# Performance work log

Measured on AMD Instinct MI355X. Metric: run time of the kernel, lower is better.

The kernel has to match this reference:

```python
import jax, jax.numpy as jnp
import numpy as np

LRELU_GAIN = np.sqrt(2.0).astype(np.float32)  # apply_activation gain for leaky_relu


def setup_inputs() -> dict:
    key = jax.random.key(0)
    ks = jax.random.split(key, 8)
    N, H, W, C_in = 8, 256, 256, 128
    num_ws, w_dim, fmaps, kernel = 16, 512, 128, 3
    return {
        "x": jax.random.normal(ks[0], (N, H, W, C_in), dtype=jnp.float32),
        "dlatents": jax.random.normal(ks[1], (N, num_ws, w_dim), dtype=jnp.float32),
        "noise": jax.random.normal(ks[2], (N, H, W, 1), dtype=jnp.float32),
        "affine_w": jax.random.normal(ks[3], (w_dim, C_in), dtype=jnp.float32),
        "affine_b": jnp.ones((C_in,), dtype=jnp.float32),  # bias_init=1
        "conv_w": jax.random.normal(ks[4], (kernel, kernel, C_in, fmaps), dtype=jnp.float32),
        "conv_b": jax.random.normal(ks[5], (fmaps,), dtype=jnp.float32),
        "noise_strength": jax.random.uniform(ks[6], (1,), dtype=jnp.float32),
        "layer_idx": 5,
    }


def reference(x, dlatents, noise, affine_w, affine_b, conv_w, conv_b, noise_strength, layer_idx):
    # --- affine (equalized-lr Linear, lr_multiplier=1): s = z @ (W/sqrt(fan_in)) + b ---
    w_dim = affine_w.shape[0]
    z = dlatents[:, layer_idx]                                   # [N, w_dim]
    s = z @ (affine_w * np.float32(1.0 / np.sqrt(w_dim))) + affine_b   # [N, C_in]

    # --- equalized-lr conv weight: w * 1/sqrt(k*k*C_in) ---
    k, _, cin, cout = conv_w.shape
    w = conv_w * np.float32(1.0 / np.sqrt(k * k * cin))          # [k,k,Cin,Cout]

    # --- demodulation coefficient d[n,o] = rsqrt(sum_{k,k,i} (w*s)^2 + eps) ---
    d = jax.lax.rsqrt(jnp.einsum('hwio,ni->no', jnp.square(w), jnp.square(s)) + 1e-8)  # [N, Cout]

    # --- non-fused modconv: modulate input, shared conv, demodulate output ---
    xm = x * s[:, None, None, :]                                 # [N,H,W,Cin]
    y = jax.lax.conv_general_dilated(
        xm, w, window_strides=(1, 1), padding='SAME',
        dimension_numbers=('NHWC', 'HWIO', 'NHWC'))              # [N,H,W,Cout]
    y = y * d[:, None, None, :]

    # --- noise injection, bias, activation (leaky_relu 0.2 with sqrt(2) gain) ---
    y = y + noise_strength[0] * noise
    y = y + conv_b
    return jax.nn.leaky_relu(y, negative_slope=0.2) * LRELU_GAIN
```

## Files before the change

### kernel.cpp

```cpp
#include <hip/hip_runtime.h>

typedef unsigned short u16;
typedef unsigned int   u32;
typedef __bf16 v8bf __attribute__((ext_vector_type(8)));
typedef float  v4f  __attribute__((ext_vector_type(4)));

#define INV_SQRT_W   0.044194173824159216f
#define INV_SQRT_KKC 0.029462782549439483f
#define LRELU_GAIN   1.4142135623730951f

__device__ __forceinline__ u16 f2bf(float f) {
    u32 u = __float_as_uint(f);
    u = (u + 0x7fffu + ((u >> 16) & 1u)) >> 16;
    return (u16)u;
}

__global__ void k_s(const float* __restrict__ dlat,
                    const float* __restrict__ aw,
                    const float* __restrict__ ab,
                    const int*   __restrict__ lidx,
                    float* __restrict__ s_out)
{
    const int n   = blockIdx.x;
    const int tid = threadIdx.x;
    const int i   = tid & 127, kh = tid >> 7;
    const int li  = lidx[0];
    const float* z = dlat + (n * 16 + li) * 512 + kh * 256;
    const float* a = aw + kh * 256 * 128 + i;
    float a0 = 0.f, a1 = 0.f, a2 = 0.f, a3 = 0.f;
    for (int k = 0; k < 256; k += 4) {
        a0 += z[k + 0] * a[(k + 0) * 128];
        a1 += z[k + 1] * a[(k + 1) * 128];
        a2 += z[k + 2] * a[(k + 2) * 128];
        a3 += z[k + 3] * a[(k + 3) * 128];
    }
    __shared__ float part[256];
    part[tid] = a0 + a1 + a2 + a3;
    __syncthreads();
    if (tid < 128)
        s_out[n * 128 + i] = (part[i] + part[i + 128]) * INV_SQRT_W + ab[i];
}

__global__ void k_w2(const float* __restrict__ cw, float* __restrict__ W2)
{
    const int idx = blockIdx.x * 256 + threadIdx.x;
    float acc = 0.f;
    #pragma unroll
    for (int t = 0; t < 9; ++t) {
        float w = cw[t * 16384 + idx];
        acc += w * w;
    }
    W2[idx] = acc * (INV_SQRT_KKC * INV_SQRT_KKC);
}

__global__ void k_d(const float* __restrict__ W2,
                    const float* __restrict__ s_buf,
                    float* __restrict__ d_out)
{
    const int n = blockIdx.x;
    const int o = threadIdx.x;
    __shared__ float s2[128];
    float sv = s_buf[n * 128 + o];
    s2[o] = sv * sv;
    __syncthreads();
    float acc = 1e-8f;
    #pragma unroll 4
    for (int i = 0; i < 128; ++i)
        acc += W2[i * 128 + o] * s2[i];
    d_out[n * 128 + o] = 1.0f / sqrtf(acc);
}

__global__ void k_wmod(const float* __restrict__ cw,
                       const float* __restrict__ s_buf,
                       const float* __restrict__ d_buf,
                       u16* __restrict__ wmod)
{
    const int b   = blockIdx.x;
    const int n   = b / 36;
    const int s   = b - n * 36;
    const int q4  = s / 9;
    const int r   = s - q4 * 9;
    const int tw  = r / 3, th = r - tw * 3;
    const int tap = th * 3 + tw;
    const int cibase = q4 * 32;
    const int tid = threadIdx.x;
    __shared__ float ssh[32], dsh[128];
    if (tid < 32)  ssh[tid] = s_buf[n * 128 + cibase + tid] * INV_SQRT_KKC;
    if (tid < 128) dsh[tid] = d_buf[n * 128 + tid];
    __syncthreads();
    u16* wt = wmod + ((size_t)b << 12);
    #pragma unroll
    for (int rep = 0; rep < 2; ++rep) {
        int t2   = rep * 256 + tid;
        int g    = t2 >> 7;
        int cout = t2 & 127;
        float dv = dsh[cout];
        u32 pk[4];
        #pragma unroll
        for (int jj = 0; jj < 4; ++jj) {
            int cl = g * 8 + jj * 2;
            float v0 = cw[((tap * 128 + cibase + cl) << 7) + cout]     * ssh[cl]     * dv;
            float v1 = cw[((tap * 128 + cibase + cl + 1) << 7) + cout] * ssh[cl + 1] * dv;
            pk[jj] = (u32)f2bf(v0) | ((u32)f2bf(v1) << 16);
        }
        *(uint4*)&wt[(g << 10) + (cout << 3)] = *(uint4*)pk;
    }
}

template<int T>
__device__ __forceinline__ void conv_step(const u16* __restrict__ bp,
                                          const u16* a_base,
                                          v8bf af[6], v8bf bfP[2][4],
                                          v4f acc[4][4])
{
    constexpr int q4 = T / 9, rr = T % 9, tw = rr / 3, th = rr % 3;
    constexpr int slot = T & 1;
    if constexpr (th == 0) {
        #pragma unroll
        for (int r = 0; r < 6; ++r)
            af[r] = *(const v8bf*)(a_base + q4 * 5824 + (r * 18 + tw) * 8);
    }
    #pragma unroll
    for (int mi = 0; mi < 4; ++mi)
        #pragma unroll
        for (int ni = 0; ni < 4; ++ni)
            acc[mi][ni] = __builtin_amdgcn_mfma_f32_16x16x32_bf16(
                af[mi + th], bfP[slot][ni], acc[mi][ni], 0, 0, 0);
    if constexpr (T + 2 < 36) {
        #pragma unroll
        for (int ni = 0; ni < 4; ++ni)
            bfP[slot][ni] = *(const v8bf*)(bp + (T + 2) * 4096 + ni * 128);
    }
}

__global__ __launch_bounds__(256, 3) void k_conv(
    const float* __restrict__ x,
    const float* __restrict__ noise,
    const float* __restrict__ conv_b,
    const float* __restrict__ nstr,
    const u16*   __restrict__ wmod,
    float* __restrict__ out)
{
    __shared__ __align__(16) u16 xs[23296];

    const int bid0 = blockIdx.x;
    const int bid  = ((bid0 & 7) << 9) + (bid0 >> 3);
    const int n  = bid >> 9;
    const int hb = (bid >> 4) & 31;
    const int wb = bid & 15;
    const int h0 = hb << 3, w0 = wb << 4;

    const int tid  = threadIdx.x;
    const int lane = tid & 63;
    const int wid  = tid >> 6;
    const int wm   = wid >> 1;
    const int wq   = wid & 1;
    const int lr   = lane & 15;
    const int kg   = lane >> 4;

    const float* xbase = x + ((size_t)n << 16) * 128;
    const u16* const b_base = wmod + (size_t)n * 147456 + kg * 1024 + (wq * 64 + lr) * 8;

    v8bf bfP[2][4];
    #pragma unroll
    for (int t2 = 0; t2 < 2; ++t2)
        #pragma unroll
        for (int ni = 0; ni < 4; ++ni)
            bfP[t2][ni] = *(const v8bf*)(b_base + t2 * 4096 + ni * 128);

    for (int t = tid; t < 2880; t += 256) {
        int g = t & 15, q = t >> 4;
        int rr_ = q / 18, cc = q - rr_ * 18;
        int gh = h0 + rr_ - 1, gw = w0 + cc - 1;
        float v0=0.f,v1=0.f,v2=0.f,v3=0.f,v4=0.f,v5=0.f,v6=0.f,v7=0.f;
        if ((unsigned)gh < 256u && (unsigned)gw < 256u) {
            const float* src = xbase + (size_t)((gh << 8) + gw) * 128 + (g << 3);
            float4 fa = *(const float4*)(src);
            float4 fb = *(const float4*)(src + 4);
            v0=fa.x; v1=fa.y; v2=fa.z; v3=fa.w; v4=fb.x; v5=fb.y; v6=fb.z; v7=fb.w;
        }
        v8bf pk;
        pk[0]=(__bf16)v0; pk[1]=(__bf16)v1; pk[2]=(__bf16)v2; pk[3]=(__bf16)v3;
        pk[4]=(__bf16)v4; pk[5]=(__bf16)v5; pk[6]=(__bf16)v6; pk[7]=(__bf16)v7;
        *(v8bf*)&xs[g * 1456 + q * 8] = pk;
    }

    v4f acc[4][4];
    #pragma unroll
    for (int a = 0; a < 4; ++a)
        #pragma unroll
        for (int b2 = 0; b2 < 4; ++b2) {
            v4f zz = {0.f, 0.f, 0.f, 0.f};
            acc[a][b2] = zz;
        }

    const u16* const a_base = &xs[kg * 1456 + (wm * 72 + lr) * 8];

    __syncthreads();

    v8bf af[6];
    conv_step< 0>(b_base, a_base, af, bfP, acc);
    conv_step< 1>(b_base, a_base, af, bfP, acc);
    conv_step< 2>(b_base, a_base, af, bfP, acc);
    conv_step< 3>(b_base, a_base, af, bfP, acc);
    conv_step< 4>(b_base, a_base, af, bfP, acc);
    conv_step< 5>(b_base, a_base, af, bfP, acc);
    conv_step< 6>(b_base, a_base, af, bfP, acc);
    conv_step< 7>(b_base, a_base, af, bfP, acc);
    conv_step< 8>(b_base, a_base, af, bfP, acc);
    conv_step< 9>(b_base, a_base, af, bfP, acc);
    conv_step<10>(b_base, a_base, af, bfP, acc);
    conv_step<11>(b_base, a_base, af, bfP, acc);
    conv_step<12>(b_base, a_base, af, bfP, acc);
    conv_step<13>(b_base, a_base, af, bfP, acc);
    conv_step<14>(b_base, a_base, af, bfP, acc);
    conv_step<15>(b_base, a_base, af, bfP, acc);
    conv_step<16>(b_base, a_base, af, bfP, acc);
    conv_step<17>(b_base, a_base, af, bfP, acc);
    conv_step<18>(b_base, a_base, af, bfP, acc);
    conv_step<19>(b_base, a_base, af, bfP, acc);
    conv_step<20>(b_base, a_base, af, bfP, acc);
    conv_step<21>(b_base, a_base, af, bfP, acc);
    conv_step<22>(b_base, a_base, af, bfP, acc);
    conv_step<23>(b_base, a_base, af, bfP, acc);
    conv_step<24>(b_base, a_base, af, bfP, acc);
    conv_step<25>(b_base, a_base, af, bfP, acc);
    conv_step<26>(b_base, a_base, af, bfP, acc);
    conv_step<27>(b_base, a_base, af, bfP, acc);
    conv_step<28>(b_base, a_base, af, bfP, acc);
    conv_step<29>(b_base, a_base, af, bfP, acc);
    conv_step<30>(b_base, a_base, af, bfP, acc);
    conv_step<31>(b_base, a_base, af, bfP, acc);
    conv_step<32>(b_base, a_base, af, bfP, acc);
    conv_step<33>(b_base, a_base, af, bfP, acc);
    conv_step<34>(b_base, a_base, af, bfP, acc);
    conv_step<35>(b_base, a_base, af, bfP, acc);

    const float ns = nstr[0];
    float cb4[4];
    #pragma unroll
    for (int ni = 0; ni < 4; ++ni)
        cb4[ni] = conv_b[wq * 64 + ni * 16 + lr];
    #pragma unroll
    for (int mi = 0; mi < 4; ++mi) {
        const int h = h0 + wm * 4 + mi;
        #pragma unroll
        for (int j = 0; j < 4; ++j) {
            const int w  = w0 + kg * 4 + j;
            const float nz = noise[((n << 8) + h) * 256 + w] * ns;
            float* orow = out + (size_t)((((n << 8) + h) << 8) + w) * 128;
            #pragma unroll
            for (int ni = 0; ni < 4; ++ni) {
                const int cout = wq * 64 + ni * 16 + lr;
                float v = acc[mi][ni][j] + nz + cb4[ni];
                v = (v < 0.f ? 0.2f * v : v) * LRELU_GAIN;
                orow[cout] = v;
            }
        }
    }
}

extern "C" void kernel_launch(void* const* d_in, const int* in_sizes, int n_in,
                              void* d_out, int out_size, void* d_ws, size_t ws_size,
                              hipStream_t stream) {
    const float* x     = (const float*)d_in[0];
    const float* dlat  = (const float*)d_in[1];
    const float* noise = (const float*)d_in[2];
    const float* aw    = (const float*)d_in[3];
    const float* ab    = (const float*)d_in[4];
    const float* cw    = (const float*)d_in[5];
    const float* cb    = (const float*)d_in[6];
    const float* nstr  = (const float*)d_in[7];
    const int*   lidx  = (const int*)d_in[8];
    float* out = (float*)d_out;

    float* s_buf = (float*)d_ws;
    float* d_buf = (float*)((char*)d_ws + 4096);
    float* W2    = (float*)((char*)d_ws + 8192);
    u16*   wmod  = (u16*)((char*)d_ws + 8192);

    k_w2  <<<64,  256, 0, stream>>>(cw, W2);
    k_s   <<<8,   256, 0, stream>>>(dlat, aw, ab, lidx, s_buf);
    k_d   <<<8,   128, 0, stream>>>(W2, s_buf, d_buf);
    k_wmod<<<288, 256, 0, stream>>>(cw, s_buf, d_buf, wmod);
    k_conv<<<4096,256, 0, stream>>>(x, noise, cb, nstr, wmod, out);
}
```

Baseline: 225.5 us.

## Overlap second-half input tile staging with first-half MFMA steps

The input halo tile is split into two channel halves. Only the first half is loaded before the barrier. The second half's global loads and LDS writes are interleaved with the first 18 MFMA steps, and a second barrier follows before the remaining steps. A-fragments are now reloaded from LDS every step instead of being cached across three taps, and MFMA blocks are wrapped in s_setprio. This aims to hide input load latency behind compute, at the cost of more LDS reads and an extra barrier.

```diff
diff --git a/kernel.cpp b/kernel.cpp
--- a/kernel.cpp
+++ b/kernel.cpp
@@ -107,25 +107,34 @@
     }
 }
 
+__device__ __forceinline__ void pack_write(u16* dst, float4 a, float4 b) {
+    v8bf pk;
+    pk[0] = (__bf16)a.x; pk[1] = (__bf16)a.y; pk[2] = (__bf16)a.z; pk[3] = (__bf16)a.w;
+    pk[4] = (__bf16)b.x; pk[5] = (__bf16)b.y; pk[6] = (__bf16)b.z; pk[7] = (__bf16)b.w;
+    *(v8bf*)dst = pk;
+}
+
 template<int T>
 __device__ __forceinline__ void conv_step(const u16* __restrict__ bp,
                                           const u16* a_base,
-                                          v8bf af[6], v8bf bfP[2][4],
+                                          v8bf bfP[2][4],
                                           v4f acc[4][4])
 {
     constexpr int q4 = T / 9, rr = T % 9, tw = rr / 3, th = rr % 3;
+    constexpr int h  = q4 >> 1, q2 = q4 & 1;
     constexpr int slot = T & 1;
-    if constexpr (th == 0) {
-        #pragma unroll
-        for (int r = 0; r < 6; ++r)
-            af[r] = *(const v8bf*)(a_base + q4 * 5824 + (r * 18 + tw) * 8);
-    }
+    v8bf af[4];
+    #pragma unroll
+    for (int mi = 0; mi < 4; ++mi)
+        af[mi] = *(const v8bf*)(a_base + h * 11648 + q2 * 5824 + ((mi + th) * 18 + tw) * 8);
+    __builtin_amdgcn_s_setprio(1);
     #pragma unroll
     for (int mi = 0; mi < 4; ++mi)
         #pragma unroll
         for (int ni = 0; ni < 4; ++ni)
             acc[mi][ni] = __builtin_amdgcn_mfma_f32_16x16x32_bf16(
-                af[mi + th], bfP[slot][ni], acc[mi][ni], 0, 0, 0);
+                af[mi], bfP[slot][ni], acc[mi][ni], 0, 0, 0);
+    __builtin_amdgcn_s_setprio(0);
     if constexpr (T + 2 < 36) {
         #pragma unroll
         for (int ni = 0; ni < 4; ++ni)
@@ -160,6 +169,18 @@
 
     const float* xbase = x + ((size_t)n << 16) * 128;
     const u16* const b_base = wmod + (size_t)n * 147456 + kg * 1024 + (wq * 64 + lr) * 8;
+    const float4 f4z = {0.f, 0.f, 0.f, 0.f};
+
+    int off[6];
+    #pragma unroll
+    for (int j = 0; j < 6; ++j) {
+        int t  = tid + j * 256;
+        int q  = t >> 3, g = t & 7;
+        int rr = q / 18, cc = q - rr * 18;
+        int gh = h0 + rr - 1, gw = w0 + cc - 1;
+        bool ok = (t < 1440) && ((unsigned)gh < 256u) && ((unsigned)gw < 256u);
+        off[j] = ok ? (((gh << 8) + gw) * 128 + g * 8) : -1;
+    }
 
     v8bf bfP[2][4];
     #pragma unroll
@@ -168,21 +189,23 @@
         for (int ni = 0; ni < 4; ++ni)
             bfP[t2][ni] = *(const v8bf*)(b_base + t2 * 4096 + ni * 128);
 
-    for (int t = tid; t < 2880; t += 256) {
-        int g = t & 15, q = t >> 4;
-        int rr_ = q / 18, cc = q - rr_ * 18;
-        int gh = h0 + rr_ - 1, gw = w0 + cc - 1;
-        float v0=0.f,v1=0.f,v2=0.f,v3=0.f,v4=0.f,v5=0.f,v6=0.f,v7=0.f;
-        if ((unsigned)gh < 256u && (unsigned)gw < 256u) {
-            const float* src = xbase + (size_t)((gh << 8) + gw) * 128 + (g << 3);
-            float4 fa = *(const float4*)(src);
-            float4 fb = *(const float4*)(src + 4);
-            v0=fa.x; v1=fa.y; v2=fa.z; v3=fa.w; v4=fb.x; v5=fb.y; v6=fb.z; v7=fb.w;
-        }
-        v8bf pk;
-        pk[0]=(__bf16)v0; pk[1]=(__bf16)v1; pk[2]=(__bf16)v2; pk[3]=(__bf16)v3;
-        pk[4]=(__bf16)v4; pk[5]=(__bf16)v5; pk[6]=(__bf16)v6; pk[7]=(__bf16)v7;
-        *(v8bf*)&xs[g * 1456 + q * 8] = pk;
+    #define LD0(J, A, B_) { bool ok = off[J] >= 0;                                  \
+        const float* sp = xbase + (ok ? off[J] : 0);                                \
+        A  = ok ? *(const float4*)sp       : f4z;                                   \
+        B_ = ok ? *(const float4*)(sp + 4) : f4z; }
+    #define LD1(J, A, B_) { bool ok = off[J] >= 0;                                  \
+        const float* sp = xbase + (ok ? off[J] : 0) + 64;                           \
+        A  = ok ? *(const float4*)sp       : f4z;                                   \
+        B_ = ok ? *(const float4*)(sp + 4) : f4z; }
+    #define WR(J, HALF, A, B_) {                                                    \
+        int t = tid + (J) * 256; int q = t >> 3, g = t & 7;                         \
+        pack_write(&xs[(HALF) * 11648 + g * 1456 + q * 8], A, B_); }
+
+    {
+        float4 a0,b0,a1,b1,a2,b2,a3,b3,a4,b4,a5,b5;
+        LD0(0,a0,b0) LD0(1,a1,b1) LD0(2,a2,b2) LD0(3,a3,b3) LD0(4,a4,b4) LD0(5,a5,b5)
+        WR(0,0,a0,b0) WR(1,0,a1,b1) WR(2,0,a2,b2) WR(3,0,a3,b3) WR(4,0,a4,b4)
+        if (tid < 160) WR(5,0,a5,b5)
     }
 
     v4f acc[4][4];
@@ -198,43 +221,59 @@
 
     __syncthreads();
 
-    v8bf af[6];
-    conv_step< 0>(b_base, a_base, af, bfP, acc);
-    conv_step< 1>(b_base, a_base, af, bfP, acc);
-    conv_step< 2>(b_base, a_base, af, bfP, acc);
-    conv_step< 3>(b_base, a_base, af, bfP, acc);
-    conv_step< 4>(b_base, a_base, af, bfP, acc);
-    conv_step< 5>(b_base, a_base, af, bfP, acc);
-    conv_step< 6>(b_base, a_base, af, bfP, acc);
-    conv_step< 7>(b_base, a_base, af, bfP, acc);
-    conv_step< 8>(b_base, a_base, af, bfP, acc);
-    conv_step< 9>(b_base, a_base, af, bfP, acc);
-    conv_step<10>(b_base, a_base, af, bfP, acc);
-    conv_step<11>(b_base, a_base, af, bfP, acc);
-    conv_step<12>(b_base, a_base, af, bfP, acc);
-    conv_step<13>(b_base, a_base, af, bfP, acc);
-    conv_step<14>(b_base, a_base, af, bfP, acc);
-    conv_step<15>(b_base, a_base, af, bfP, acc);
-    conv_step<16>(b_base, a_base, af, bfP, acc);
-    conv_step<17>(b_base, a_base, af, bfP, acc);
-    conv_step<18>(b_base, a_base, af, bfP, acc);
-    conv_step<19>(b_base, a_base, af, bfP, acc);
-    conv_step<20>(b_base, a_base, af, bfP, acc);
-    conv_step<21>(b_base, a_base, af, bfP, acc);
-    conv_step<22>(b_base, a_base, af, bfP, acc);
-    conv_step<23>(b_base, a_base, af, bfP, acc);
-    conv_step<24>(b_base, a_base, af, bfP, acc);
-    conv_step<25>(b_base, a_base, af, bfP, acc);
-    conv_step<26>(b_base, a_base, af, bfP, acc);
-    conv_step<27>(b_base, a_base, af, bfP, acc);
-    conv_step<28>(b_base, a_base, af, bfP, acc);
-    conv_step<29>(b_base, a_base, af, bfP, acc);
-    conv_step<30>(b_base, a_base, af, bfP, acc);
-    conv_step<31>(b_base, a_base, af, bfP, acc);
-    conv_step<32>(b_base, a_base, af, bfP, acc);
-    conv_step<33>(b_base, a_base, af, bfP, acc);
-    conv_step<34>(b_base, a_base, af, bfP, acc);
-    conv_step<35>(b_base, a_base, af, bfP, acc);
+    float4 sa0, sb0, sa1, sb1;
+    LD1(0, sa0, sb0) LD1(1, sa1, sb1)
+
+    conv_step< 0>(b_base, a_base, bfP, acc);
+    conv_step< 1>(b_base, a_base, bfP, acc);
+    conv_step< 2>(b_base, a_base, bfP, acc);
+    conv_step< 3>(b_base, a_base, bfP, acc);
+    conv_step< 4>(b_base, a_base, bfP, acc);
+    conv_step< 5>(b_base, a_base, bfP, acc);
+
+    WR(0, 1, sa0, sb0) WR(1, 1, sa1, sb1)
+    LD1(2, sa0, sb0) LD1(3, sa1, sb1)
+
+    conv_step< 6>(b_base, a_base, bfP, acc);
+    conv_step< 7>(b_base, a_base, bfP, acc);
+    conv_step< 8>(b_base, a_base, bfP, acc);
+    conv_step< 9>(b_base, a_base, bfP, acc);
+    conv_step<10>(b_base, a_base, bfP, acc);
+    conv_step<11>(b_base, a_base, bfP, acc);
+
+    WR(2, 1, sa0, sb0) WR(3, 1, sa1, sb1)
+    LD1(4, sa0, sb0) LD1(5, sa1, sb1)
+
+    conv_step<12>(b_base, a_base, bfP, acc);
+    conv_step<13>(b_base, a_base, bfP, acc);
+    conv_step<14>(b_base, a_base, bfP, acc);
+    conv_step<15>(b_base, a_base, bfP, acc);
+    conv_step<16>(b_base, a_base, bfP, acc);
+    conv_step<17>(b_base, a_base, bfP, acc);
+
+    WR(4, 1, sa0, sb0)
+    if (tid < 160) WR(5, 1, sa1, sb1)
+
+    __syncthreads();
+
+    conv_step<18>(b_base, a_base, bfP, acc);
+    conv_step<19>(b_base, a_base, bfP, acc);
+    conv_step<20>(b_base, a_base, bfP, acc);
+    conv_step<21>(b_base, a_base, bfP, acc);
+    conv_step<22>(b_base, a_base, bfP, acc);
+    conv_step<23>(b_base, a_base, bfP, acc);
+    conv_step<24>(b_base, a_base, bfP, acc);
+    conv_step<25>(b_base, a_base, bfP, acc);
+    conv_step<26>(b_base, a_base, bfP, acc);
+    conv_step<27>(b_base, a_base, bfP, acc);
+    conv_step<28>(b_base, a_base, bfP, acc);
+    conv_step<29>(b_base, a_base, bfP, acc);
+    conv_step<30>(b_base, a_base, bfP, acc);
+    conv_step<31>(b_base, a_base, bfP, acc);
+    conv_step<32>(b_base, a_base, bfP, acc);
+    conv_step<33>(b_base, a_base, bfP, acc);
+    conv_step<34>(b_base, a_base, bfP, acc);
+    conv_step<35>(b_base, a_base, bfP, acc);
 
     const float ns = nstr[0];
     float cb4[4];
```

Result: slower. 366.2 us (+62.4%).

## Stage modulated weights through LDS with async global_load_lds triple buffering

Applied to the files above, without the earlier changes.

Each wave used to read its B fragments of the modulated weights straight from global memory into registers, double-buffered. Now the block copies each tap's weight tile into a three-slot LDS ring with global_load_lds, syncing with a waitcnt and a barrier every step. This shares weight loads across the four waves and frees registers. The cost is a barrier per step, extra LDS (which lowers occupancy to 2 blocks via launch_bounds), and hand-written vmcnt waits that could be fragile.

```diff
diff --git a/kernel.cpp b/kernel.cpp
--- a/kernel.cpp
+++ b/kernel.cpp
@@ -13,6 +13,12 @@
     u32 u = __float_as_uint(f);
     u = (u + 0x7fffu + ((u >> 16) & 1u)) >> 16;
     return (u16)u;
+}
+
+__device__ __forceinline__ void glds16(const u16* g, u16* l) {
+    __builtin_amdgcn_global_load_lds(
+        (const __attribute__((address_space(1))) void*)g,
+        (__attribute__((address_space(3))) void*)l, 16, 0, 0);
 }
 
 __global__ void k_s(const float* __restrict__ dlat,
@@ -108,32 +114,46 @@
 }
 
 template<int T>
-__device__ __forceinline__ void conv_step(const u16* __restrict__ bp,
+__device__ __forceinline__ void conv_step(const u16* __restrict__ wn,
+                                          u16* __restrict__ bsh,
                                           const u16* a_base,
-                                          v8bf af[6], v8bf bfP[2][4],
-                                          v4f acc[4][4])
+                                          const u16* b_lane,
+                                          v8bf af[6], v4f acc[4][4],
+                                          int wid, int lane)
 {
     constexpr int q4 = T / 9, rr = T % 9, tw = rr / 3, th = rr % 3;
-    constexpr int slot = T & 1;
+    constexpr int slot = T % 3;
+    if constexpr (T < 35) asm volatile("s_waitcnt vmcnt(2)" ::: "memory");
+    else                  asm volatile("s_waitcnt vmcnt(0)" ::: "memory");
+    __builtin_amdgcn_s_barrier();
+    asm volatile("" ::: "memory");
+    v8bf bf[4];
+    #pragma unroll
+    for (int ni = 0; ni < 4; ++ni)
+        bf[ni] = *(const v8bf*)(b_lane + slot * 4096 + ni * 128);
     if constexpr (th == 0) {
         #pragma unroll
         for (int r = 0; r < 6; ++r)
             af[r] = *(const v8bf*)(a_base + q4 * 5824 + (r * 18 + tw) * 8);
     }
+    if constexpr (T + 2 < 36) {
+        constexpr int ns = (T + 2) % 3;
+        #pragma unroll
+        for (int t = 0; t < 2; ++t) {
+            int chunk = wid + (t << 2);
+            glds16(wn + (T + 2) * 4096 + (chunk << 9) + (lane << 3),
+                   &bsh[ns * 4096 + (chunk << 9) + (lane << 3)]);
+        }
+    }
     #pragma unroll
     for (int mi = 0; mi < 4; ++mi)
         #pragma unroll
         for (int ni = 0; ni < 4; ++ni)
             acc[mi][ni] = __builtin_amdgcn_mfma_f32_16x16x32_bf16(
-                af[mi + th], bfP[slot][ni], acc[mi][ni], 0, 0, 0);
-    if constexpr (T + 2 < 36) {
-        #pragma unroll
-        for (int ni = 0; ni < 4; ++ni)
-            bfP[slot][ni] = *(const v8bf*)(bp + (T + 2) * 4096 + ni * 128);
-    }
-}
-
-__global__ __launch_bounds__(256, 3) void k_conv(
+                af[mi + th], bf[ni], acc[mi][ni], 0, 0, 0);
+}
+
+__global__ __launch_bounds__(256, 2) void k_conv(
     const float* __restrict__ x,
     const float* __restrict__ noise,
     const float* __restrict__ conv_b,
@@ -142,6 +162,7 @@
     float* __restrict__ out)
 {
     __shared__ __align__(16) u16 xs[23296];
+    __shared__ __align__(16) u16 bsh[12288];
 
     const int bid0 = blockIdx.x;
     const int bid  = ((bid0 & 7) << 9) + (bid0 >> 3);
@@ -159,14 +180,7 @@
     const int kg   = lane >> 4;
 
     const float* xbase = x + ((size_t)n << 16) * 128;
-    const u16* const b_base = wmod + (size_t)n * 147456 + kg * 1024 + (wq * 64 + lr) * 8;
-
-    v8bf bfP[2][4];
-    #pragma unroll
-    for (int t2 = 0; t2 < 2; ++t2)
-        #pragma unroll
-        for (int ni = 0; ni < 4; ++ni)
-            bfP[t2][ni] = *(const v8bf*)(b_base + t2 * 4096 + ni * 128);
+    const u16* wn = wmod + (size_t)n * 147456;
 
     for (int t = tid; t < 2880; t += 256) {
         int g = t & 15, q = t >> 4;
@@ -185,6 +199,15 @@
         *(v8bf*)&xs[g * 1456 + q * 8] = pk;
     }
 
+    #pragma unroll
+    for (int s0 = 0; s0 < 2; ++s0)
+        #pragma unroll
+        for (int t = 0; t < 2; ++t) {
+            int chunk = wid + (t << 2);
+            glds16(wn + s0 * 4096 + (chunk << 9) + (lane << 3),
+                   &bsh[s0 * 4096 + (chunk << 9) + (lane << 3)]);
+        }
+
     v4f acc[4][4];
     #pragma unroll
     for (int a = 0; a < 4; ++a)
@@ -195,46 +218,47 @@
         }
 
     const u16* const a_base = &xs[kg * 1456 + (wm * 72 + lr) * 8];
-
-    __syncthreads();
+    const u16* const b_lane = &bsh[kg * 1024 + (wq * 64 + lr) * 8];
+
+    asm volatile("s_waitcnt lgkmcnt(0)" ::: "memory");
 
     v8bf af[6];
-    conv_step< 0>(b_base, a_base, af, bfP, acc);
-    conv_step< 1>(b_base, a_base, af, bfP, acc);
-    conv_step< 2>(b_base, a_base, af, bfP, acc);
-    conv_step< 3>(b_base, a_base, af, bfP, acc);
-    conv_step< 4>(b_base, a_base, af, bfP, acc);
-    conv_step< 5>(b_base, a_base, af, bfP, acc);
-    conv_step< 6>(b_base, a_base, af, bfP, acc);
-    conv_step< 7>(b_base, a_base, af, bfP, acc);
-    conv_step< 8>(b_base, a_base, af, bfP, acc);
-    conv_step< 9>(b_base, a_base, af, bfP, acc);
-    conv_step<10>(b_base, a_base, af, bfP, acc);
-    conv_step<11>(b_base, a_base, af, bfP, acc);
-    conv_step<12>(b_base, a_base, af, bfP, acc);
-    conv_step<13>(b_base, a_base, af, bfP, acc);
-    conv_step<14>(b_base, a_base, af, bfP, acc);
-    conv_step<15>(b_base, a_base, af, bfP, acc);
-    conv_step<16>(b_base, a_base, af, bfP, acc);
-    conv_step<17>(b_base, a_base, af, bfP, acc);
-    conv_step<18>(b_base, a_base, af, bfP, acc);
-    conv_step<19>(b_base, a_base, af, bfP, acc);
-    conv_step<20>(b_base, a_base, af, bfP, acc);
-    conv_step<21>(b_base, a_base, af, bfP, acc);
-    conv_step<22>(b_base, a_base, af, bfP, acc);
-    conv_step<23>(b_base, a_base, af, bfP, acc);
-    conv_step<24>(b_base, a_base, af, bfP, acc);
-    conv_step<25>(b_base, a_base, af, bfP, acc);
-    conv_step<26>(b_base, a_base, af, bfP, acc);
-    conv_step<27>(b_base, a_base, af, bfP, acc);
-    conv_step<28>(b_base, a_base, af, bfP, acc);
-    conv_step<29>(b_base, a_base, af, bfP, acc);
-    conv_step<30>(b_base, a_base, af, bfP, acc);
-    conv_step<31>(b_base, a_base, af, bfP, acc);
-    conv_step<32>(b_base, a_base, af, bfP, acc);
-    conv_step<33>(b_base, a_base, af, bfP, acc);
-    conv_step<34>(b_base, a_base, af, bfP, acc);
-    conv_step<35>(b_base, a_base, af, bfP, acc);
+    conv_step< 0>(wn, bsh, a_base, b_lane, af, acc, wid, lane);
+    conv_step< 1>(wn, bsh, a_base, b_lane, af, acc, wid, lane);
+    conv_step< 2>(wn, bsh, a_base, b_lane, af, acc, wid, lane);
+    conv_step< 3>(wn, bsh, a_base, b_lane, af, acc, wid, lane);
+    conv_step< 4>(wn, bsh, a_base, b_lane, af, acc, wid, lane);
+    conv_step< 5>(wn, bsh, a_base, b_lane, af, acc, wid, lane);
+    conv_step< 6>(wn, bsh, a_base, b_lane, af, acc, wid, lane);
+    conv_step< 7>(wn, bsh, a_base, b_lane, af, acc, wid, lane);
+    conv_step< 8>(wn, bsh, a_base, b_lane, af, acc, wid, lane);
+    conv_step< 9>(wn, bsh, a_base, b_lane, af, acc, wid, lane);
+    conv_step<10>(wn, bsh, a_base, b_lane, af, acc, wid, lane);
+    conv_step<11>(wn, bsh, a_base, b_lane, af, acc, wid, lane);
+    conv_step<12>(wn, bsh, a_base, b_lane, af, acc, wid, lane);
+    conv_step<13>(wn, bsh, a_base, b_lane, af, acc, wid, lane);
+    conv_step<14>(wn, bsh, a_base, b_lane, af, acc, wid, lane);
+    conv_step<15>(wn, bsh, a_base, b_lane, af, acc, wid, lane);
+    conv_step<16>(wn, bsh, a_base, b_lane, af, acc, wid, lane);
+    conv_step<17>(wn, bsh, a_base, b_lane, af, acc, wid, lane);
+    conv_step<18>(wn, bsh, a_base, b_lane, af, acc, wid, lane);
+    conv_step<19>(wn, bsh, a_base, b_lane, af, acc, wid, lane);
+    conv_step<20>(wn, bsh, a_base, b_lane, af, acc, wid, lane);
+    conv_step<21>(wn, bsh, a_base, b_lane, af, acc, wid, lane);
+    conv_step<22>(wn, bsh, a_base, b_lane, af, acc, wid, lane);
+    conv_step<23>(wn, bsh, a_base, b_lane, af, acc, wid, lane);
+    conv_step<24>(wn, bsh, a_base, b_lane, af, acc, wid, lane);
+    conv_step<25>(wn, bsh, a_base, b_lane, af, acc, wid, lane);
+    conv_step<26>(wn, bsh, a_base, b_lane, af, acc, wid, lane);
+    conv_step<27>(wn, bsh, a_base, b_lane, af, acc, wid, lane);
+    conv_step<28>(wn, bsh, a_base, b_lane, af, acc, wid, lane);
+    conv_step<29>(wn, bsh, a_base, b_lane, af, acc, wid, lane);
+    conv_step<30>(wn, bsh, a_base, b_lane, af, acc, wid, lane);
+    conv_step<31>(wn, bsh, a_base, b_lane, af, acc, wid, lane);
+    conv_step<32>(wn, bsh, a_base, b_lane, af, acc, wid, lane);
+    conv_step<33>(wn, bsh, a_base, b_lane, af, acc, wid, lane);
+    conv_step<34>(wn, bsh, a_base, b_lane, af, acc, wid, lane);
+    conv_step<35>(wn, bsh, a_base, b_lane, af, acc, wid, lane);
 
     const float ns = nstr[0];
     float cb4[4];
```

Measured after the change: 241.0 us. 6.9% more time.

## Make conv kernel persistent with triple-buffered per-channel-quarter input pipeline

Applied to the files above, without the earlier changes.

Turns the conv kernel into a persistent one: 768 blocks each walk 5-6 consecutive output tiles instead of launching one block per tile. Each tile's input halo is split into four channel-quarter chunks that rotate through a three-slot LDS buffer. Global loads for the next chunk, or the next tile's first chunk, are issued during the MFMAs on the current chunk, overlapping the input fetch with compute and cutting shared memory. The cost is more barriers per tile, extra registers holding staged loads, and an uneven tile count across blocks.

```diff
diff --git a/kernel.cpp b/kernel.cpp
--- a/kernel.cpp
+++ b/kernel.cpp
@@ -107,29 +107,28 @@
     }
 }
 
-template<int T>
-__device__ __forceinline__ void conv_step(const u16* __restrict__ bp,
-                                          const u16* a_base,
+template<int S>
+__device__ __forceinline__ void conv_step(const u16* __restrict__ bl,
+                                          const u16* a_cur,
                                           v8bf af[6], v8bf bfP[2][4],
                                           v4f acc[4][4])
 {
-    constexpr int q4 = T / 9, rr = T % 9, tw = rr / 3, th = rr % 3;
-    constexpr int slot = T & 1;
+    constexpr int ST = S % 9, tw = ST / 3, th = ST % 3, par = S & 1;
     if constexpr (th == 0) {
         #pragma unroll
-        for (int r = 0; r < 6; ++r)
-            af[r] = *(const v8bf*)(a_base + q4 * 5824 + (r * 18 + tw) * 8);
+        for (int rr = 0; rr < 6; ++rr)
+            af[rr] = *(const v8bf*)(a_cur + (rr * 18 + tw) * 8);
     }
     #pragma unroll
     for (int mi = 0; mi < 4; ++mi)
         #pragma unroll
         for (int ni = 0; ni < 4; ++ni)
             acc[mi][ni] = __builtin_amdgcn_mfma_f32_16x16x32_bf16(
-                af[mi + th], bfP[slot][ni], acc[mi][ni], 0, 0, 0);
-    if constexpr (T + 2 < 36) {
+                af[mi + th], bfP[par][ni], acc[mi][ni], 0, 0, 0);
+    if constexpr (S + 2 < 36) {
         #pragma unroll
         for (int ni = 0; ni < 4; ++ni)
-            bfP[slot][ni] = *(const v8bf*)(bp + (T + 2) * 4096 + ni * 128);
+            bfP[par][ni] = *(const v8bf*)(bl + (S + 2) * 4096 + ni * 128);
     }
 }
 
@@ -141,14 +140,12 @@
     const u16*   __restrict__ wmod,
     float* __restrict__ out)
 {
-    __shared__ __align__(16) u16 xs[23296];
-
-    const int bid0 = blockIdx.x;
-    const int bid  = ((bid0 & 7) << 9) + (bid0 >> 3);
-    const int n  = bid >> 9;
-    const int hb = (bid >> 4) & 31;
-    const int wb = bid & 15;
-    const int h0 = hb << 3, w0 = wb << 4;
+    __shared__ __align__(16) u16 xs[17472];
+
+    const int r0 = blockIdx.x;
+    const int r  = ((r0 & 7) * 96) + (r0 >> 3);
+    const int nt = 5 + (((r % 3) == 0) ? 1 : 0);
+    const int t0 = 5 * r + (r + 2) / 3;
 
     const int tid  = threadIdx.x;
     const int lane = tid & 63;
@@ -158,103 +155,182 @@
     const int lr   = lane & 15;
     const int kg   = lane >> 4;
 
-    const float* xbase = x + ((size_t)n << 16) * 128;
-    const u16* const b_base = wmod + (size_t)n * 147456 + kg * 1024 + (wq * 64 + lr) * 8;
-
-    v8bf bfP[2][4];
-    #pragma unroll
-    for (int t2 = 0; t2 < 2; ++t2)
-        #pragma unroll
-        for (int ni = 0; ni < 4; ++ni)
-            bfP[t2][ni] = *(const v8bf*)(b_base + t2 * 4096 + ni * 128);
-
-    for (int t = tid; t < 2880; t += 256) {
-        int g = t & 15, q = t >> 4;
-        int rr_ = q / 18, cc = q - rr_ * 18;
-        int gh = h0 + rr_ - 1, gw = w0 + cc - 1;
-        float v0=0.f,v1=0.f,v2=0.f,v3=0.f,v4=0.f,v5=0.f,v6=0.f,v7=0.f;
-        if ((unsigned)gh < 256u && (unsigned)gw < 256u) {
-            const float* src = xbase + (size_t)((gh << 8) + gw) * 128 + (g << 3);
-            float4 fa = *(const float4*)(src);
-            float4 fb = *(const float4*)(src + 4);
-            v0=fa.x; v1=fa.y; v2=fa.z; v3=fa.w; v4=fb.x; v5=fb.y; v6=fb.z; v7=fb.w;
-        }
-        v8bf pk;
-        pk[0]=(__bf16)v0; pk[1]=(__bf16)v1; pk[2]=(__bf16)v2; pk[3]=(__bf16)v3;
-        pk[4]=(__bf16)v4; pk[5]=(__bf16)v5; pk[6]=(__bf16)v6; pk[7]=(__bf16)v7;
-        *(v8bf*)&xs[g * 1456 + q * 8] = pk;
-    }
-
-    v4f acc[4][4];
-    #pragma unroll
-    for (int a = 0; a < 4; ++a)
-        #pragma unroll
-        for (int b2 = 0; b2 < 4; ++b2) {
-            v4f zz = {0.f, 0.f, 0.f, 0.f};
-            acc[a][b2] = zz;
-        }
-
-    const u16* const a_base = &xs[kg * 1456 + (wm * 72 + lr) * 8];
-
-    __syncthreads();
-
-    v8bf af[6];
-    conv_step< 0>(b_base, a_base, af, bfP, acc);
-    conv_step< 1>(b_base, a_base, af, bfP, acc);
-    conv_step< 2>(b_base, a_base, af, bfP, acc);
-    conv_step< 3>(b_base, a_base, af, bfP, acc);
-    conv_step< 4>(b_base, a_base, af, bfP, acc);
-    conv_step< 5>(b_base, a_base, af, bfP, acc);
-    conv_step< 6>(b_base, a_base, af, bfP, acc);
-    conv_step< 7>(b_base, a_base, af, bfP, acc);
-    conv_step< 8>(b_base, a_base, af, bfP, acc);
-    conv_step< 9>(b_base, a_base, af, bfP, acc);
-    conv_step<10>(b_base, a_base, af, bfP, acc);
-    conv_step<11>(b_base, a_base, af, bfP, acc);
-    conv_step<12>(b_base, a_base, af, bfP, acc);
-    conv_step<13>(b_base, a_base, af, bfP, acc);
-    conv_step<14>(b_base, a_base, af, bfP, acc);
-    conv_step<15>(b_base, a_base, af, bfP, acc);
-    conv_step<16>(b_base, a_base, af, bfP, acc);
-    conv_step<17>(b_base, a_base, af, bfP, acc);
-    conv_step<18>(b_base, a_base, af, bfP, acc);
-    conv_step<19>(b_base, a_base, af, bfP, acc);
-    conv_step<20>(b_base, a_base, af, bfP, acc);
-    conv_step<21>(b_base, a_base, af, bfP, acc);
-    conv_step<22>(b_base, a_base, af, bfP, acc);
-    conv_step<23>(b_base, a_base, af, bfP, acc);
-    conv_step<24>(b_base, a_base, af, bfP, acc);
-    conv_step<25>(b_base, a_base, af, bfP, acc);
-    conv_step<26>(b_base, a_base, af, bfP, acc);
-    conv_step<27>(b_base, a_base, af, bfP, acc);
-    conv_step<28>(b_base, a_base, af, bfP, acc);
-    conv_step<29>(b_base, a_base, af, bfP, acc);
-    conv_step<30>(b_base, a_base, af, bfP, acc);
-    conv_step<31>(b_base, a_base, af, bfP, acc);
-    conv_step<32>(b_base, a_base, af, bfP, acc);
-    conv_step<33>(b_base, a_base, af, bfP, acc);
-    conv_step<34>(b_base, a_base, af, bfP, acc);
-    conv_step<35>(b_base, a_base, af, bfP, acc);
+    int s_q[3], s_g[3], s_rr[3], s_cc[3]; bool s_v[3];
+    #pragma unroll
+    for (int j = 0; j < 3; ++j) {
+        int tj = tid + j * 256;
+        s_v[j]  = (tj < 720);
+        s_q[j]  = tj >> 2;
+        s_g[j]  = tj & 3;
+        s_rr[j] = s_q[j] / 18;
+        s_cc[j] = s_q[j] - s_rr[j] * 18;
+    }
+
+    const int a_off = kg * 1456 + (wm * 72 + lr) * 8;
+    const int b_off = kg * 1024 + (wq * 64 + lr) * 8;
+
+    float4 sa[3], sb[3];
+    const float4 f4z = {0.f, 0.f, 0.f, 0.f};
+
+#define ISSUE(Q4, H0, W0, XB, EN)                                                  \
+    {                                                                              \
+        _Pragma("unroll")                                                          \
+        for (int j = 0; j < 3; ++j) {                                              \
+            int gh = (H0) + s_rr[j] - 1, gw = (W0) + s_cc[j] - 1;                  \
+            bool ok = (EN) && s_v[j] && (unsigned)gh < 256u && (unsigned)gw < 256u;\
+            const float* sp = (XB) + (ok ? (size_t)(((gh << 8) + gw) * 128         \
+                                   + (Q4) * 32 + s_g[j] * 8) : (size_t)0);         \
+            sa[j] = ok ? *(const float4*)sp       : f4z;                           \
+            sb[j] = ok ? *(const float4*)(sp + 4) : f4z;                           \
+        }                                                                          \
+    }
+
+#define COMMIT(SLOT, EN)                                                           \
+    if (EN) {                                                                      \
+        _Pragma("unroll")                                                          \
+        for (int j = 0; j < 3; ++j) if (s_v[j]) {                                  \
+            v8bf pk;                                                               \
+            pk[0]=(__bf16)sa[j].x; pk[1]=(__bf16)sa[j].y;                          \
+            pk[2]=(__bf16)sa[j].z; pk[3]=(__bf16)sa[j].w;                          \
+            pk[4]=(__bf16)sb[j].x; pk[5]=(__bf16)sb[j].y;                          \
+            pk[6]=(__bf16)sb[j].z; pk[7]=(__bf16)sb[j].w;                          \
+            *(v8bf*)&xs[(SLOT) * 5824 + s_g[j] * 1456 + s_q[j] * 8] = pk;          \
+        }                                                                          \
+    }
+
+#define QBAR()                                                                     \
+    asm volatile("s_waitcnt lgkmcnt(0)" ::: "memory");                             \
+    __builtin_amdgcn_s_barrier();                                                  \
+    asm volatile("" ::: "memory");
+
+    int slot = 0;
+
+    {
+        const int tile = t0;
+        const int pn  = tile >> 9;
+        const int ph0 = ((tile >> 4) & 31) << 3;
+        const int pw0 = (tile & 15) << 4;
+        const float* pxb = x + ((size_t)pn << 16) * 128;
+        ISSUE(0, ph0, pw0, pxb, true)
+        COMMIT(0, true)
+        QBAR()
+    }
 
     const float ns = nstr[0];
     float cb4[4];
     #pragma unroll
     for (int ni = 0; ni < 4; ++ni)
         cb4[ni] = conv_b[wq * 64 + ni * 16 + lr];
-    #pragma unroll
-    for (int mi = 0; mi < 4; ++mi) {
-        const int h = h0 + wm * 4 + mi;
-        #pragma unroll
-        for (int j = 0; j < 4; ++j) {
-            const int w  = w0 + kg * 4 + j;
-            const float nz = noise[((n << 8) + h) * 256 + w] * ns;
-            float* orow = out + (size_t)((((n << 8) + h) << 8) + w) * 128;
+
+    for (int t = 0; t < nt; ++t) {
+        const int tile = t0 + t;
+        const int n  = tile >> 9;
+        const int h0 = ((tile >> 4) & 31) << 3;
+        const int w0 = (tile & 15) << 4;
+        const float* xb = x + ((size_t)n << 16) * 128;
+        const u16* bl = wmod + (size_t)n * 147456 + b_off;
+
+        const bool hn = (t + 1 < nt);
+        const int tile2 = hn ? (tile + 1) : tile;
+        const int n2  = tile2 >> 9;
+        const int h02 = ((tile2 >> 4) & 31) << 3;
+        const int w02 = (tile2 & 15) << 4;
+        const float* xb2 = x + ((size_t)n2 << 16) * 128;
+
+        v8bf bfP[2][4];
+        #pragma unroll
+        for (int p = 0; p < 2; ++p)
             #pragma unroll
-            for (int ni = 0; ni < 4; ++ni) {
-                const int cout = wq * 64 + ni * 16 + lr;
-                float v = acc[mi][ni][j] + nz + cb4[ni];
-                v = (v < 0.f ? 0.2f * v : v) * LRELU_GAIN;
-                orow[cout] = v;
+            for (int ni = 0; ni < 4; ++ni)
+                bfP[p][ni] = *(const v8bf*)(bl + p * 4096 + ni * 128);
+
+        v4f acc[4][4];
+        #pragma unroll
+        for (int a = 0; a < 4; ++a)
+            #pragma unroll
+            for (int b2 = 0; b2 < 4; ++b2) {
+                v4f zz = {0.f, 0.f, 0.f, 0.f};
+                acc[a][b2] = zz;
+            }
+
+        v8bf af[6];
+        int snxt = slot + 1; if (snxt == 3) snxt = 0;
+        const u16* a_cur = &xs[slot * 5824 + a_off];
+
+        ISSUE(1, h0, w0, xb, true)
+        conv_step< 0>(bl, a_cur, af, bfP, acc);
+        conv_step< 1>(bl, a_cur, af, bfP, acc);
+        conv_step< 2>(bl, a_cur, af, bfP, acc);
+        conv_step< 3>(bl, a_cur, af, bfP, acc);
+        conv_step< 4>(bl, a_cur, af, bfP, acc);
+        conv_step< 5>(bl, a_cur, af, bfP, acc);
+        conv_step< 6>(bl, a_cur, af, bfP, acc);
+        COMMIT(snxt, true)
+        conv_step< 7>(bl, a_cur, af, bfP, acc);
+        conv_step< 8>(bl, a_cur, af, bfP, acc);
+        QBAR()
+        slot = snxt; snxt = slot + 1; if (snxt == 3) snxt = 0;
+        a_cur = &xs[slot * 5824 + a_off];
+
+        ISSUE(2, h0, w0, xb, true)
+        conv_step< 9>(bl, a_cur, af, bfP, acc);
+        conv_step<10>(bl, a_cur, af, bfP, acc);
+        conv_step<11>(bl, a_cur, af, bfP, acc);
+        conv_step<12>(bl, a_cur, af, bfP, acc);
+        conv_step<13>(bl, a_cur, af, bfP, acc);
+        conv_step<14>(bl, a_cur, af, bfP, acc);
+        conv_step<15>(bl, a_cur, af, bfP, acc);
+        COMMIT(snxt, true)
+        conv_step<16>(bl, a_cur, af, bfP, acc);
+        conv_step<17>(bl, a_cur, af, bfP, acc);
+        QBAR()
+        slot = snxt; snxt = slot + 1; if (snxt == 3) snxt = 0;
+        a_cur = &xs[slot * 5824 + a_off];
+
+        ISSUE(3, h0, w0, xb, true)
+        conv_step<18>(bl, a_cur, af, bfP, acc);
+        conv_step<19>(bl, a_cur, af, bfP, acc);
+        conv_step<20>(bl, a_cur, af, bfP, acc);
+        conv_step<21>(bl, a_cur, af, bfP, acc);
+        conv_step<22>(bl, a_cur, af, bfP, acc);
+        conv_step<23>(bl, a_cur, af, bfP, acc);
+        conv_step<24>(bl, a_cur, af, bfP, acc);
+        COMMIT(snxt, true)
+        conv_step<25>(bl, a_cur, af, bfP, acc);
+        conv_step<26>(bl, a_cur, af, bfP, acc);
+        QBAR()
+        slot = snxt; snxt = slot + 1; if (snxt == 3) snxt = 0;
+        a_cur = &xs[slot * 5824 + a_off];
+
+        ISSUE(0, h02, w02, xb2, hn)
+        conv_step<27>(bl, a_cur, af, bfP, acc);
+        conv_step<28>(bl, a_cur, af, bfP, acc);
+        conv_step<29>(bl, a_cur, af, bfP, acc);
+        conv_step<30>(bl, a_cur, af, bfP, acc);
+        conv_step<31>(bl, a_cur, af, bfP, acc);
+        conv_step<32>(bl, a_cur, af, bfP, acc);
+        conv_step<33>(bl, a_cur, af, bfP, acc);
+        COMMIT(snxt, hn)
+        conv_step<34>(bl, a_cur, af, bfP, acc);
+        conv_step<35>(bl, a_cur, af, bfP, acc);
+        QBAR()
+        slot = snxt;
+
+        #pragma unroll
+        for (int mi = 0; mi < 4; ++mi) {
+            const int h = h0 + wm * 4 + mi;
+            #pragma unroll
+            for (int j = 0; j < 4; ++j) {
+                const int w  = w0 + kg * 4 + j;
+                const float nz = noise[((n << 8) + h) * 256 + w] * ns;
+                float* orow = out + (size_t)((((n << 8) + h) << 8) + w) * 128;
+                #pragma unroll
+                for (int ni = 0; ni < 4; ++ni) {
+                    const int cout = wq * 64 + ni * 16 + lr;
+                    float v = acc[mi][ni][j] + nz + cb4[ni];
+                    v = (v < 0.f ? 0.2f * v : v) * LRELU_GAIN;
+                    orow[cout] = v;
+                }
             }
         }
     }
@@ -283,5 +359,5 @@
     k_s   <<<8,   256, 0, stream>>>(dlat, aw, ab, lidx, s_buf);
     k_d   <<<8,   128, 0, stream>>>(W2, s_buf, d_buf);
     k_wmod<<<288, 256, 0, stream>>>(cw, s_buf, d_buf, wmod);
-    k_conv<<<4096,256, 0, stream>>>(x, noise, cb, nstr, wmod, out);
-}
+    k_conv<<<768, 256, 0, stream>>>(x, noise, cb, nstr, wmod, out);
+}
```

Measured after the change: 306.5 us. +35.9%, slower.
